# Performance work log

Hardware: AMD Instinct MI355X
Metric: run time of the kernel (lower is better)

Reference implementation:

```python
import jax, jax.numpy as jnp
import numpy as np

B, S, DIN, DOUT = 4, 2048, 4096, 4096

def setup_inputs() -> dict:
    key = jax.random.key(0)
    k1, k2, k3 = jax.random.split(key, 3)
    inp = jax.random.normal(k1, (B, S, DIN), dtype=jnp.float16)
    # int8 quantized weights in [-127, 127]
    qweight = jax.random.randint(k2, (DOUT, DIN), -127, 128, dtype=jnp.int32).astype(jnp.int8)
    # per-output-channel scales, small positive
    qscales = (jax.random.uniform(k3, (DOUT, 1), dtype=jnp.float32) * 0.01 + 1e-4).astype(jnp.float16)
    return {"inp": inp, "qweight": qweight, "qscales": qscales}

def reference(inp, qweight, qscales):
    # Dequantize: int8 * fp16 scale -> fp16 weight [out, in] (matches torch promotion + .to(fp16))
    w = (qweight.astype(jnp.float16) * qscales).astype(jnp.float16)
    # F.linear(inp, w) = inp @ w.T ; note: bias is NOT added in the original forward
    return jnp.einsum("bsd,od->bso", inp, w)
```

## Files before the change

kernel.cpp:

```cpp
#include <hip/hip_runtime.h>
#include <stdint.h>


#define M_DIM 8192
#define N_DIM 4096
#define K_DIM 4096
#define BM 256
#define BN 256
#define BK 32
#define NKT (K_DIM / BK)

typedef _Float16 f16;
typedef f16 f16x8 __attribute__((ext_vector_type(8)));
typedef f16 f16x2 __attribute__((ext_vector_type(2)));
typedef float f32x4 __attribute__((ext_vector_type(4)));

static __device__ __forceinline__ f16x2 cvt2(float a, float b) {
  return __builtin_bit_cast(f16x2, __builtin_amdgcn_cvt_pkrtz(a, b));
}


__global__ __launch_bounds__(256) void conv_a_kernel(
    const float* __restrict__ A, f16* __restrict__ Af)
{
  const size_t stride = (size_t)gridDim.x * blockDim.x;
  size_t i = (size_t)blockIdx.x * blockDim.x + threadIdx.x;
  const size_t n8 = (size_t)M_DIM * K_DIM / 8;
  for (; i < n8; i += stride) {
    const f32x4* p = (const f32x4*)(A + i * 8);
    f32x4 v0 = p[0], v1 = p[1];
    f16x2 a = cvt2(v0.x, v0.y), b = cvt2(v0.z, v0.w);
    f16x2 c = cvt2(v1.x, v1.y), d = cvt2(v1.z, v1.w);
    *(f16x8*)(Af + i * 8) = (f16x8){a.x, a.y, b.x, b.y, c.x, c.y, d.x, d.y};
  }
}

__global__ __launch_bounds__(256) void conv_b_kernel(
    const int* __restrict__ Qw, const float* __restrict__ Sc,
    f16* __restrict__ Wf)
{
  const int o = blockIdx.x;
  const int t = threadIdx.x;
  const float s = Sc[o];
  const int* q = Qw + (size_t)o * K_DIM + t * 16;
  f16* w = Wf + (size_t)o * K_DIM + t * 16;
  #pragma unroll
  for (int h = 0; h < 2; ++h) {
    int4 u0 = *(const int4*)(q + h * 8);
    int4 u1 = *(const int4*)(q + h * 8 + 4);
    f16x2 a = cvt2((float)u0.x * s, (float)u0.y * s);
    f16x2 b = cvt2((float)u0.z * s, (float)u0.w * s);
    f16x2 c = cvt2((float)u1.x * s, (float)u1.y * s);
    f16x2 d = cvt2((float)u1.z * s, (float)u1.w * s);
    *(f16x8*)(w + h * 8) = (f16x8){a.x, a.y, b.x, b.y, c.x, c.y, d.x, d.y};
  }
}


#define BARX() __builtin_amdgcn_s_barrier()
#define SCHED0() __builtin_amdgcn_sched_barrier(0)
#define LGKM(n) do { asm volatile("s_waitcnt lgkmcnt(" #n ")" ::: "memory"); \
                     __builtin_amdgcn_sched_barrier(0); } while (0)
#define VMW(n)  do { asm volatile("s_waitcnt vmcnt(" #n ")" ::: "memory"); \
                     __builtin_amdgcn_sched_barrier(0); } while (0)

#define STAGE_A(bi, ktn) do { \
  _Pragma("unroll") \
  for (int _i = 0; _i < 2; ++_i) { \
    const f16* _g = aSrc + (size_t)((st_R + 64 * _i) * 2 + st_h) * K_DIM \
                    + (ktn) * BK + st_s * 8; \
    char* _l = (char*)&As[bi][0] + _i * 8192 + wid * 1024; \
    __builtin_amdgcn_global_load_lds( \
        (const __attribute__((address_space(1))) void*)_g, \
        (__attribute__((address_space(3))) void*)_l, 16, 0, 0); \
  } } while (0)

#define STAGE_B(bi, ktn) do { \
  _Pragma("unroll") \
  for (int _i = 0; _i < 2; ++_i) { \
    const f16* _g = bSrc + (size_t)((st_R + 64 * _i) * 2 + st_h) * K_DIM \
                    + (ktn) * BK + st_s * 8; \
    char* _l = (char*)&Bs[bi][0] + _i * 8192 + wid * 1024; \
    __builtin_amdgcn_global_load_lds( \
        (const __attribute__((address_space(1))) void*)_g, \
        (__attribute__((address_space(3))) void*)_l, 16, 0, 0); \
  } } while (0)

#define A_LDS(CB, j) (const f16x8*)((const char*)&As[CB][0] + aoff + 2048 * (j))
#define B_LDS(CB, n) (const f16x8*)((const char*)&Bs[CB][0] + boff + 4096 * (n))

#define READ_AF(dst, jb, CB) do { \
  dst[0] = *A_LDS(CB, (jb) + 0); dst[1] = *A_LDS(CB, (jb) + 1); \
  dst[2] = *A_LDS(CB, (jb) + 2); dst[3] = *A_LDS(CB, (jb) + 3); } while (0)

#define READ_BF(dst, CB) do { \
  dst[0] = *B_LDS(CB, 0); dst[1] = *B_LDS(CB, 1); \
  dst[2] = *B_LDS(CB, 2); dst[3] = *B_LDS(CB, 3); } while (0)

#define MFMA_HALF(jb, A_, B_) do { \
  __builtin_amdgcn_s_setprio(1); \
  _Pragma("unroll") \
  for (int _m = 0; _m < 4; ++_m) \
    _Pragma("unroll") \
    for (int _n = 0; _n < 4; ++_n) \
      acc[(jb) + _m][_n] = __builtin_amdgcn_mfma_f32_16x16x32_f16( \
          A_[_m], B_[_n], acc[(jb) + _m][_n], 0, 0, 0); \
  __builtin_amdgcn_s_setprio(0); } while (0)

#define TILE(KT, CB, NB, SB, BFC, BFN, M1, M2) do { \
   \
  if (M2) STAGE_A(SB, (KT) + 2); \
  READ_AF(af_bot, 4, CB); \
  BARX(); \
  LGKM(4); \
  MFMA_HALF(0, af_top, BFC); \
  BARX(); \
   \
  if (M2) { STAGE_B(SB, (KT) + 2); VMW(4); } \
  else    { VMW(0); } \
  BARX(); SCHED0(); \
  if (M1) { \
    READ_AF(af_top, 0, NB); \
    READ_BF(BFN, NB); \
    LGKM(8); \
  } else { LGKM(0); } \
  MFMA_HALF(4, af_bot, BFC); \
  BARX(); \
} while (0)

__global__ __launch_bounds__(512, 1) void w8a16_gemm_f16_kernel(
    const f16* __restrict__ Af,
    const f16* __restrict__ Wf,
    float* __restrict__ Out)
{
  __shared__ __align__(16) f16 As[4][BM * BK];
  __shared__ __align__(16) f16 Bs[4][BN * BK];

  const int t    = threadIdx.x;
  const int lane = t & 63;
  const int wid  = t >> 6;
  const int wm   = wid >> 2;
  const int wn   = wid & 3;
  const int fr   = lane & 15;
  const int qk   = lane >> 4;

  const int st_R = t >> 3;
  const int st_x = (t & 7) ^ (st_R & 7);
  const int st_h = st_x >> 2;
  const int st_s = st_x & 3;

  const int ca   = wm * 16 + fr;
  const int aoff = (ca >> 1) * 128
                 + (((((ca & 1) << 2) | qk) ^ ((ca >> 1) & 7)) << 4);
  const int cbv  = wn * 16 + fr;
  const int boff = (cbv >> 1) * 128
                 + (((((cbv & 1) << 2) | qk) ^ ((cbv >> 1) & 7)) << 4);

  const int bid = blockIdx.x;
  const int swz = (bid & 7) * 64 + (bid >> 3);
  const int tn  = swz & 15;
  const int tm  = swz >> 4;

  const f16* aSrc = Af + (size_t)tm * BM * K_DIM;
  const f16* bSrc = Wf + (size_t)tn * BN * K_DIM;

  f32x4 acc[8][4] = {};
  f16x8 af_top[4], af_bot[4], bfA[4], bfB[4];

  STAGE_A(0, 0); STAGE_B(0, 0);
  STAGE_A(1, 1); STAGE_B(1, 1);
  VMW(4);
  BARX(); SCHED0();
  READ_AF(af_top, 0, 0);
  READ_BF(bfA, 0);

  for (int kt = 0; kt < NKT - 4; kt += 4) {
    TILE(kt    , 0, 1, 2, bfA, bfB, 1, 1);
    TILE(kt + 1, 1, 2, 3, bfB, bfA, 1, 1);
    TILE(kt + 2, 2, 3, 0, bfA, bfB, 1, 1);
    TILE(kt + 3, 3, 0, 1, bfB, bfA, 1, 1);
  }
  TILE(NKT - 4, 0, 1, 2, bfA, bfB, 1, 1);
  TILE(NKT - 3, 1, 2, 3, bfB, bfA, 1, 1);
  TILE(NKT - 2, 2, 3, 0, bfA, bfB, 1, 0);
  TILE(NKT - 1, 3, 0, 1, bfB, bfA, 0, 0);

  const int fq = lane >> 4;
  #pragma unroll
  for (int mi = 0; mi < 8; ++mi) {
    const size_t row = (size_t)tm * BM + (2 * mi + wm) * 16 + fq * 4;
    #pragma unroll
    for (int ni = 0; ni < 4; ++ni) {
      const size_t col = (size_t)tn * BN + ni * 64 + wn * 16 + fr;
      #pragma unroll
      for (int r = 0; r < 4; ++r)
        Out[(row + r) * N_DIM + col] = acc[mi][ni][r];
    }
  }
}


__global__ __launch_bounds__(256) void w8a16_gemm_fb_kernel(
    const float* __restrict__ A, const int* __restrict__ Qw,
    const float* __restrict__ Sc, float* __restrict__ Out)
{
  __shared__ __align__(16) float Asf[2][128 * 32];
  __shared__ __align__(16) f16 Bsf[2][128][32];

  const int t = threadIdx.x, lane = t & 63, wid = t >> 6;
  const int wr = wid >> 1, wc = wid & 1;
  const int nwg = gridDim.x, cpx = nwg >> 3, bid = blockIdx.x;
  const int swz = (bid & 7) * cpx + (bid >> 3);
  const int tn = swz & 31, tm = swz >> 5;
  const size_t a_base = (size_t)tm * 128 * K_DIM;
  const size_t b_base = (size_t)tn * 128 * K_DIM;
  f32x4 acc[4][4] = {};
  const int a_r = t >> 3;
  const int a_slog = (t & 7) ^ ((t >> 3) & 7);

  auto stageA = [&](int buf, int kt) {
    #pragma unroll
    for (int c = 0; c < 4; ++c) {
      const float* g = A + a_base + (size_t)(c * 32 + a_r) * K_DIM + kt * 32 + a_slog * 4;
      char* l = (char*)&Asf[buf][0] + c * 4096 + wid * 1024;
      __builtin_amdgcn_global_load_lds(
          (const __attribute__((address_space(1))) void*)g,
          (__attribute__((address_space(3))) void*)l, 16, 0, 0);
    }
  };
  const int b_r = t >> 3, b_col = (t & 7) * 4;
  auto loadB = [&](int kt, int4* v) {
    #pragma unroll
    for (int c = 0; c < 4; ++c)
      v[c] = *(const int4*)(Qw + b_base + (size_t)(c * 32 + b_r) * K_DIM + kt * 32 + b_col);
  };
  auto writeB = [&](int buf, const int4* v) {
    #pragma unroll
    for (int c = 0; c < 4; ++c) {
      f16x2 lo = cvt2((float)v[c].x, (float)v[c].y);
      f16x2 hi = cvt2((float)v[c].z, (float)v[c].w);
      *(f16x2*)&Bsf[buf][c * 32 + b_r][b_col] = lo;
      *(f16x2*)&Bsf[buf][c * 32 + b_r][b_col + 2] = hi;
    }
  };
  auto compute = [&](int buf) {
    const int fr2 = lane & 15, q = lane >> 4;
    f16x8 af2[4], bf2[4];
    #pragma unroll
    for (int i = 0; i < 4; ++i) {
      const int r = wr * 64 + i * 16 + fr2;
      const float* base = &Asf[buf][0] + r * 32;
      const int s0 = q * 2;
      f32x4 a0 = *(const f32x4*)(base + ((s0 ^ (r & 7)) * 4));
      f32x4 a1 = *(const f32x4*)(base + (((s0 + 1) ^ (r & 7)) * 4));
      f16x2 p0 = cvt2(a0.x, a0.y), p1 = cvt2(a0.z, a0.w);
      f16x2 p2 = cvt2(a1.x, a1.y), p3 = cvt2(a1.z, a1.w);
      af2[i] = (f16x8){p0.x, p0.y, p1.x, p1.y, p2.x, p2.y, p3.x, p3.y};
      bf2[i] = *(const f16x8*)&Bsf[buf][wc * 64 + i * 16 + fr2][q * 8];
    }
    #pragma unroll
    for (int mi = 0; mi < 4; ++mi)
      #pragma unroll
      for (int ni = 0; ni < 4; ++ni)
        acc[mi][ni] = __builtin_amdgcn_mfma_f32_16x16x32_f16(
            af2[mi], bf2[ni], acc[mi][ni], 0, 0, 0);
  };

  { int4 b0[4]; stageA(0, 0); loadB(0, b0); writeB(0, b0); }
  __syncthreads();
  for (int kt = 0; kt < K_DIM / 32; ++kt) {
    const int buf = kt & 1;
    const bool more = (kt + 1) < K_DIM / 32;
    int4 nb[4];
    if (more) { stageA(buf ^ 1, kt + 1); loadB(kt + 1, nb); }
    compute(buf);
    if (more) writeB(buf ^ 1, nb);
    __syncthreads();
  }
  const int fr2 = lane & 15, fq = lane >> 4;
  const int cb = tn * 128 + wc * 64 + fr2;
  const int rb = tm * 128 + wr * 64 + fq * 4;
  #pragma unroll
  for (int ni = 0; ni < 4; ++ni) {
    const float s = Sc[cb + ni * 16];
    #pragma unroll
    for (int mi = 0; mi < 4; ++mi)
      #pragma unroll
      for (int r = 0; r < 4; ++r)
        Out[(size_t)(rb + mi * 16 + r) * N_DIM + (cb + ni * 16)] =
            acc[mi][ni][r] * s;
  }
}

extern "C" void kernel_launch(void* const* d_in, const int* in_sizes, int n_in,
                              void* d_out, int out_size, void* d_ws, size_t ws_size,
                              hipStream_t stream) {
  const float* A  = (const float*)d_in[0];
  const int*   Qw = (const int*)d_in[1];
  const float* Sc = (const float*)d_in[2];
  float*       Out = (float*)d_out;

  const size_t a_bytes = (size_t)M_DIM * K_DIM * sizeof(f16);
  const size_t w_bytes = (size_t)N_DIM * K_DIM * sizeof(f16);

  if (ws_size >= a_bytes + w_bytes) {
    f16* Af = (f16*)d_ws;
    f16* Wf = (f16*)((char*)d_ws + a_bytes);
    conv_a_kernel<<<2048, 256, 0, stream>>>(A, Af);
    conv_b_kernel<<<N_DIM, 256, 0, stream>>>(Qw, Sc, Wf);
    dim3 grid((M_DIM / BM) * (N_DIM / BN));
    w8a16_gemm_f16_kernel<<<grid, 512, 0, stream>>>(Af, Wf, Out);
  } else {
    dim3 grid((M_DIM / 128) * (N_DIM / 128));
    w8a16_gemm_fb_kernel<<<grid, 256, 0, stream>>>(A, Qw, Sc, Out);
  }
}
```

Before: 339.0 us.

## Load B fragments directly from global into registers, double-buffer only A in LDS

Removes B staging through shared memory: each wave now loads its B fragments straight from global memory into registers one k-tile ahead. Only A is still staged through LDS, now double-buffered instead of quad-buffered. The finely interleaved half-tile schedule with lgkm waits is replaced by a simpler per-tile loop that waits on vmcnt(0) and a barrier, and the block-to-tile swizzle is changed to favour reuse along M. This cuts LDS traffic and footprint, at the cost of uncoalesced strided global loads for B, a shallower prefetch distance, and a full memory stall every tile.

```diff
diff --git a/kernel.cpp b/kernel.cpp
--- a/kernel.cpp
+++ b/kernel.cpp
@@ -59,10 +59,8 @@
 
 #define BARX() __builtin_amdgcn_s_barrier()
 #define SCHED0() __builtin_amdgcn_sched_barrier(0)
-#define LGKM(n) do { asm volatile("s_waitcnt lgkmcnt(" #n ")" ::: "memory"); \
-                     __builtin_amdgcn_sched_barrier(0); } while (0)
-#define VMW(n)  do { asm volatile("s_waitcnt vmcnt(" #n ")" ::: "memory"); \
-                     __builtin_amdgcn_sched_barrier(0); } while (0)
+#define VMW0() do { asm volatile("s_waitcnt vmcnt(0)" ::: "memory"); \
+                    __builtin_amdgcn_sched_barrier(0); } while (0)
 
 #define STAGE_A(bi, ktn) do { \
   _Pragma("unroll") \
@@ -75,56 +73,26 @@
         (__attribute__((address_space(3))) void*)_l, 16, 0, 0); \
   } } while (0)
 
-#define STAGE_B(bi, ktn) do { \
+#define A_LDS(CB, j) (const f16x8*)((const char*)&As[CB][0] + aoff + 2048 * (j))
+
+#define TILE(KT, CURB, NXTB, BCUR, BNXT, M1) do { \
+  if (M1) { \
+    const f16* _bk = bSrc + (size_t)((KT) + 1) * BK; \
+    BNXT[0] = *(const f16x8*)(_bk + bo0); \
+    BNXT[1] = *(const f16x8*)(_bk + bo1); \
+    BNXT[2] = *(const f16x8*)(_bk + bo2); \
+    BNXT[3] = *(const f16x8*)(_bk + bo3); \
+    STAGE_A(NXTB, (KT) + 1); \
+  } \
   _Pragma("unroll") \
-  for (int _i = 0; _i < 2; ++_i) { \
-    const f16* _g = bSrc + (size_t)((st_R + 64 * _i) * 2 + st_h) * K_DIM \
-                    + (ktn) * BK + st_s * 8; \
-    char* _l = (char*)&Bs[bi][0] + _i * 8192 + wid * 1024; \
-    __builtin_amdgcn_global_load_lds( \
-        (const __attribute__((address_space(1))) void*)_g, \
-        (__attribute__((address_space(3))) void*)_l, 16, 0, 0); \
-  } } while (0)
-
-#define A_LDS(CB, j) (const f16x8*)((const char*)&As[CB][0] + aoff + 2048 * (j))
-#define B_LDS(CB, n) (const f16x8*)((const char*)&Bs[CB][0] + boff + 4096 * (n))
-
-#define READ_AF(dst, jb, CB) do { \
-  dst[0] = *A_LDS(CB, (jb) + 0); dst[1] = *A_LDS(CB, (jb) + 1); \
-  dst[2] = *A_LDS(CB, (jb) + 2); dst[3] = *A_LDS(CB, (jb) + 3); } while (0)
-
-#define READ_BF(dst, CB) do { \
-  dst[0] = *B_LDS(CB, 0); dst[1] = *B_LDS(CB, 1); \
-  dst[2] = *B_LDS(CB, 2); dst[3] = *B_LDS(CB, 3); } while (0)
-
-#define MFMA_HALF(jb, A_, B_) do { \
-  __builtin_amdgcn_s_setprio(1); \
+  for (int _j = 0; _j < 8; ++_j) af[_j] = *A_LDS(CURB, _j); \
   _Pragma("unroll") \
-  for (int _m = 0; _m < 4; ++_m) \
+  for (int _m = 0; _m < 8; ++_m) \
     _Pragma("unroll") \
     for (int _n = 0; _n < 4; ++_n) \
-      acc[(jb) + _m][_n] = __builtin_amdgcn_mfma_f32_16x16x32_f16( \
-          A_[_m], B_[_n], acc[(jb) + _m][_n], 0, 0, 0); \
-  __builtin_amdgcn_s_setprio(0); } while (0)
-
-#define TILE(KT, CB, NB, SB, BFC, BFN, M1, M2) do { \
-   \
-  if (M2) STAGE_A(SB, (KT) + 2); \
-  READ_AF(af_bot, 4, CB); \
-  BARX(); \
-  LGKM(4); \
-  MFMA_HALF(0, af_top, BFC); \
-  BARX(); \
-   \
-  if (M2) { STAGE_B(SB, (KT) + 2); VMW(4); } \
-  else    { VMW(0); } \
-  BARX(); SCHED0(); \
-  if (M1) { \
-    READ_AF(af_top, 0, NB); \
-    READ_BF(BFN, NB); \
-    LGKM(8); \
-  } else { LGKM(0); } \
-  MFMA_HALF(4, af_bot, BFC); \
+      acc[_m][_n] = __builtin_amdgcn_mfma_f32_16x16x32_f16( \
+          af[_m], BCUR[_n], acc[_m][_n], 0, 0, 0); \
+  VMW0(); \
   BARX(); \
 } while (0)
 
@@ -133,8 +101,7 @@
     const f16* __restrict__ Wf,
     float* __restrict__ Out)
 {
-  __shared__ __align__(16) f16 As[4][BM * BK];
-  __shared__ __align__(16) f16 Bs[4][BN * BK];
+  __shared__ __align__(16) f16 As[2][BM * BK];
 
   const int t    = threadIdx.x;
   const int lane = t & 63;
@@ -152,38 +119,41 @@
   const int ca   = wm * 16 + fr;
   const int aoff = (ca >> 1) * 128
                  + (((((ca & 1) << 2) | qk) ^ ((ca >> 1) & 7)) << 4);
-  const int cbv  = wn * 16 + fr;
-  const int boff = (cbv >> 1) * 128
-                 + (((((cbv & 1) << 2) | qk) ^ ((cbv >> 1) & 7)) << 4);
+
+  const uint32_t bo0 = (uint32_t)((0 * 64 + wn * 16 + fr) * K_DIM + qk * 8);
+  const uint32_t bo1 = (uint32_t)((1 * 64 + wn * 16 + fr) * K_DIM + qk * 8);
+  const uint32_t bo2 = (uint32_t)((2 * 64 + wn * 16 + fr) * K_DIM + qk * 8);
+  const uint32_t bo3 = (uint32_t)((3 * 64 + wn * 16 + fr) * K_DIM + qk * 8);
 
   const int bid = blockIdx.x;
   const int swz = (bid & 7) * 64 + (bid >> 3);
-  const int tn  = swz & 15;
-  const int tm  = swz >> 4;
+  const int tn  = swz >> 5;
+  const int tm  = swz & 31;
 
   const f16* aSrc = Af + (size_t)tm * BM * K_DIM;
   const f16* bSrc = Wf + (size_t)tn * BN * K_DIM;
 
   f32x4 acc[8][4] = {};
-  f16x8 af_top[4], af_bot[4], bfA[4], bfB[4];
-
-  STAGE_A(0, 0); STAGE_B(0, 0);
-  STAGE_A(1, 1); STAGE_B(1, 1);
-  VMW(4);
-  BARX(); SCHED0();
-  READ_AF(af_top, 0, 0);
-  READ_BF(bfA, 0);
-
-  for (int kt = 0; kt < NKT - 4; kt += 4) {
-    TILE(kt    , 0, 1, 2, bfA, bfB, 1, 1);
-    TILE(kt + 1, 1, 2, 3, bfB, bfA, 1, 1);
-    TILE(kt + 2, 2, 3, 0, bfA, bfB, 1, 1);
-    TILE(kt + 3, 3, 0, 1, bfB, bfA, 1, 1);
-  }
-  TILE(NKT - 4, 0, 1, 2, bfA, bfB, 1, 1);
-  TILE(NKT - 3, 1, 2, 3, bfB, bfA, 1, 1);
-  TILE(NKT - 2, 2, 3, 0, bfA, bfB, 1, 0);
-  TILE(NKT - 1, 3, 0, 1, bfB, bfA, 0, 0);
+  f16x8 af[8], bA[4], bB[4];
+
+  {
+    const f16* _bk = bSrc;
+    bA[0] = *(const f16x8*)(_bk + bo0);
+    bA[1] = *(const f16x8*)(_bk + bo1);
+    bA[2] = *(const f16x8*)(_bk + bo2);
+    bA[3] = *(const f16x8*)(_bk + bo3);
+  }
+  STAGE_A(0, 0);
+  VMW0();
+  BARX();
+  SCHED0();
+
+  for (int kt = 0; kt < NKT - 2; kt += 2) {
+    TILE(kt,     0, 1, bA, bB, 1);
+    TILE(kt + 1, 1, 0, bB, bA, 1);
+  }
+  TILE(NKT - 2, 0, 1, bA, bB, 1);
+  TILE(NKT - 1, 1, 0, bB, bA, 0);
 
   const int fq = lane >> 4;
   #pragma unroll
```

After: 488.3 us. 44.0% more time.
